# Kernel tuning notes

Hardware: AMD Instinct MI355X
Metric: run time of the kernel (lower is better)

## Reference

```python
import jax, jax.numpy as jnp
import numpy as np

GROUP_SIZE = 128  # K-rows sharing one dequant scale


def _dequant(B, s):
    """Unpack int4 (uint4b8: value = nibble - 8) from packed int32 and apply group scales.
    B: [K//8, N] int32, 8 nibbles per word along K (nibble i -> k = 8*row + i).
    s: [K//GROUP_SIZE, N] float scales.
    Returns W: [K, N] float.
    """
    Kp, N = B.shape
    K = Kp * 8
    shifts = (jnp.arange(8, dtype=jnp.int32) * 4)
    # [Kp, 8, N] nibbles -> [K, N]
    nib = (B[:, None, :] >> shifts[None, :, None]) & 0xF
    w = nib.reshape(K, N).astype(s.dtype) - 8.0
    # per-group scaling: groups of GROUP_SIZE consecutive K rows
    w = (w.reshape(K // GROUP_SIZE, GROUP_SIZE, N) * s[:, None, :]).reshape(K, N)
    return w


def setup_inputs() -> dict:
    key = jax.random.key(0)
    k1, k2, k3 = jax.random.split(key, 3)
    M, K, N = 64, 8192, 8192
    x = jax.random.normal(k1, (M, K), dtype=jnp.float32)
    B = jax.random.randint(k2, (K // 8, N), 0, 2147483647, dtype=jnp.int32)
    s = jax.random.uniform(k3, (K // GROUP_SIZE, N), dtype=jnp.float32) * 0.02
    return {"x": x, "B": B, "s": s}


def reference(x, B, s):
    # machete_mm: fused int4 dequant + GEMM; here expressed as dequant then matmul
    w = _dequant(B, s)          # [K, N]
    out = x @ w                 # [M, N]
    return out
```

## Files before the change

kernel.cpp:

```cpp
#include <hip/hip_runtime.h>

typedef _Float16 half2v __attribute__((ext_vector_type(2)));
typedef _Float16 half8  __attribute__((ext_vector_type(8)));
typedef float    floatx4 __attribute__((ext_vector_type(4)));

#define M_DIM 64
#define K_DIM 8192
#define N_DIM 8192
#define NT 64
#define KSPLIT 4

__global__ __launch_bounds__(256) void permute_x_kernel(
        const float* __restrict__ x, _Float16* __restrict__ xp) {
    int t = blockIdx.x * 256 + threadIdx.x;
    const float* src = x + (size_t)t * 8;
    float4 a = *(const float4*)(src);
    float4 b = *(const float4*)(src + 4);
    union { _Float16 h[8]; float4 f; } u;
    u.h[0] = (_Float16)a.x; u.h[1] = (_Float16)b.x;
    u.h[2] = (_Float16)a.y; u.h[3] = (_Float16)b.y;
    u.h[4] = (_Float16)a.z; u.h[5] = (_Float16)b.z;
    u.h[6] = (_Float16)a.w; u.h[7] = (_Float16)b.w;
    *(float4*)(xp + (size_t)t * 8) = u.f;
}

__device__ __forceinline__ half2v dq_pair(unsigned int bits, half2v sub, half2v sc) {
    union { unsigned int u; half2v h; } cv;
    cv.u = bits;
    return (cv.h - sub) * sc;
}

__global__ __launch_bounds__(256, 2) void machete_mm_kernel(
        const _Float16* __restrict__ xp,
        const unsigned int* __restrict__ Bq,
        const float* __restrict__ s,
        float* __restrict__ out) {
    __shared__ float red[4][M_DIM][NT];

    const int tid  = threadIdx.x;
    const int w    = tid >> 6;
    const int lane = tid & 63;
    const int c    = lane & 15;
    const int q    = lane >> 4;
    const int n0   = blockIdx.x * NT;
    const int ci   = blockIdx.y * 4 + w;
    const int kb   = ci * (K_DIM / (KSPLIT * 4));

    const int ncol = n0 + 4 * c;

    floatx4 acc[4][4];
    #pragma unroll
    for (int i = 0; i < 4; ++i)
        #pragma unroll
        for (int j = 0; j < 4; ++j) acc[i][j] = (floatx4)0.0f;

    const unsigned int* bptr = Bq + (size_t)((kb >> 3) + q) * N_DIM + ncol;
    const _Float16*     aptr = xp + (size_t)c * K_DIM + kb + q * 8;

    const half2v c1032 = { (_Float16)1032.0f, (_Float16)1032.0f };

    #pragma unroll
    for (int g = 0; g < 4; ++g) {
        const int gg = (kb >> 7) + g;
        const float4 s4 = *(const float4*)(s + (size_t)gg * N_DIM + ncol);
        half2v s2[4];
        s2[0] = (half2v){ (_Float16)s4.x, (_Float16)s4.x };
        s2[1] = (half2v){ (_Float16)s4.y, (_Float16)s4.y };
        s2[2] = (half2v){ (_Float16)s4.z, (_Float16)s4.z };
        s2[3] = (half2v){ (_Float16)s4.w, (_Float16)s4.w };

        #pragma unroll
        for (int st = 0; st < 4; ++st) {
            half8 afr[4];
            #pragma unroll
            for (int mt = 0; mt < 4; ++mt)
                afr[mt] = *(const half8*)(aptr + (size_t)mt * 16 * K_DIM);

            union { uint4 v; unsigned int a[4]; } bv;
            bv.v = *(const uint4*)bptr;

            #pragma unroll
            for (int t = 0; t < 4; ++t) {
                const unsigned int wd = bv.a[t];
                union { half2v h2[4]; half8 h8; } bf;
                bf.h2[0] = dq_pair(( wd        & 0x000F000Fu) | 0x64006400u, c1032, s2[t]);
                bf.h2[1] = dq_pair(((wd >> 4)  & 0x000F000Fu) | 0x64006400u, c1032, s2[t]);
                bf.h2[2] = dq_pair(((wd >> 8)  & 0x000F000Fu) | 0x64006400u, c1032, s2[t]);
                bf.h2[3] = dq_pair(((wd >> 12) & 0x000F000Fu) | 0x64006400u, c1032, s2[t]);
                #pragma unroll
                for (int mt = 0; mt < 4; ++mt)
                    acc[mt][t] = __builtin_amdgcn_mfma_f32_16x16x32_f16(
                        afr[mt], bf.h8, acc[mt][t], 0, 0, 0);
            }
            aptr += 32;
            bptr += (size_t)4 * N_DIM;
        }
    }

    #pragma unroll
    for (int mt = 0; mt < 4; ++mt)
        #pragma unroll
        for (int t = 0; t < 4; ++t)
            #pragma unroll
            for (int r = 0; r < 4; ++r)
                red[w][mt * 16 + q * 4 + r][4 * c + t] = acc[mt][t][r];
    __syncthreads();

    #pragma unroll
    for (int i = 0; i < 16; ++i) {
        int idx = i * 256 + tid;
        int m = idx >> 6, nl = idx & 63;
        float v = red[0][m][nl] + red[1][m][nl] + red[2][m][nl] + red[3][m][nl];
        atomicAdd(out + (size_t)m * N_DIM + n0 + nl, v);
    }
}

extern "C" void kernel_launch(void* const* d_in, const int* in_sizes, int n_in,
                              void* d_out, int out_size, void* d_ws, size_t ws_size,
                              hipStream_t stream) {
    const float*        x  = (const float*)d_in[0];
    const unsigned int* Bq = (const unsigned int*)d_in[1];
    const float*        sc = (const float*)d_in[2];
    float* out    = (float*)d_out;
    _Float16* xp  = (_Float16*)d_ws;

    hipMemsetAsync(d_out, 0, (size_t)M_DIM * N_DIM * sizeof(float), stream);
    permute_x_kernel<<<dim3((M_DIM * K_DIM / 8) / 256), 256, 0, stream>>>(x, xp);
    machete_mm_kernel<<<dim3(N_DIM / NT, KSPLIT), 256, 0, stream>>>(xp, Bq, sc, out);
}
```

Before: 101.2 us.

## Software-pipeline B/A loads and replace atomic split-K with partial buffer reduction

The main loop is flattened into 16 steps, with B words prefetched two steps ahead through a triple buffer and A fragments prefetched one step ahead. This hides global load latency behind the MFMA and dequant work. The atomicAdd split-K epilogue and the output memset are replaced by plain stores of per-split partials into workspace, followed by a separate reduce kernel. The shared reduction buffer is halved and padded, which lowers LDS use and bank conflicts but adds an extra launch and partial-buffer traffic.

```diff
diff --git a/kernel.cpp b/kernel.cpp
--- a/kernel.cpp
+++ b/kernel.cpp
@@ -8,7 +8,7 @@
 #define K_DIM 8192
 #define N_DIM 8192
 #define NT 64
-#define KSPLIT 4
+#define KSB 4
 
 __global__ __launch_bounds__(256) void permute_x_kernel(
         const float* __restrict__ x, _Float16* __restrict__ xp) {
@@ -34,8 +34,8 @@
         const _Float16* __restrict__ xp,
         const unsigned int* __restrict__ Bq,
         const float* __restrict__ s,
-        float* __restrict__ out) {
-    __shared__ float red[4][M_DIM][NT];
+        float* __restrict__ partial) {
+    __shared__ float red[4][32][65];
 
     const int tid  = threadIdx.x;
     const int w    = tid >> 6;
@@ -44,7 +44,7 @@
     const int q    = lane >> 4;
     const int n0   = blockIdx.x * NT;
     const int ci   = blockIdx.y * 4 + w;
-    const int kb   = ci * (K_DIM / (KSPLIT * 4));
+    const int kb   = ci * (K_DIM / (KSB * 4));
 
     const int ncol = n0 + 4 * c;
 
@@ -54,65 +54,99 @@
         #pragma unroll
         for (int j = 0; j < 4; ++j) acc[i][j] = (floatx4)0.0f;
 
+    const half2v c1032 = { (_Float16)1032.0f, (_Float16)1032.0f };
+    half2v s2g[4][4];
+    #pragma unroll
+    for (int g = 0; g < 4; ++g) {
+        const float4 s4 = *(const float4*)(s + (size_t)((kb >> 7) + g) * N_DIM + ncol);
+        s2g[g][0] = (half2v){ (_Float16)s4.x, (_Float16)s4.x };
+        s2g[g][1] = (half2v){ (_Float16)s4.y, (_Float16)s4.y };
+        s2g[g][2] = (half2v){ (_Float16)s4.z, (_Float16)s4.z };
+        s2g[g][3] = (half2v){ (_Float16)s4.w, (_Float16)s4.w };
+    }
+
     const unsigned int* bptr = Bq + (size_t)((kb >> 3) + q) * N_DIM + ncol;
     const _Float16*     aptr = xp + (size_t)c * K_DIM + kb + q * 8;
 
-    const half2v c1032 = { (_Float16)1032.0f, (_Float16)1032.0f };
+    uint4 bbuf[3];
+    half8 abuf[2][4];
+    bbuf[0] = *(const uint4*)bptr; bptr += (size_t)4 * N_DIM;
+    bbuf[1] = *(const uint4*)bptr; bptr += (size_t)4 * N_DIM;
+    #pragma unroll
+    for (int mt = 0; mt < 4; ++mt)
+        abuf[0][mt] = *(const half8*)(aptr + (size_t)mt * 16 * K_DIM);
 
     #pragma unroll
-    for (int g = 0; g < 4; ++g) {
-        const int gg = (kb >> 7) + g;
-        const float4 s4 = *(const float4*)(s + (size_t)gg * N_DIM + ncol);
-        half2v s2[4];
-        s2[0] = (half2v){ (_Float16)s4.x, (_Float16)s4.x };
-        s2[1] = (half2v){ (_Float16)s4.y, (_Float16)s4.y };
-        s2[2] = (half2v){ (_Float16)s4.z, (_Float16)s4.z };
-        s2[3] = (half2v){ (_Float16)s4.w, (_Float16)s4.w };
+    for (int st = 0; st < 16; ++st) {
+        if (st < 14) {
+            bbuf[(st + 2) % 3] = *(const uint4*)bptr;
+            bptr += (size_t)4 * N_DIM;
+        }
+        if (st < 15) {
+            #pragma unroll
+            for (int mt = 0; mt < 4; ++mt)
+                abuf[(st + 1) & 1][mt] =
+                    *(const half8*)(aptr + 32 + (size_t)mt * 16 * K_DIM);
+        }
+
+        union { uint4 v; unsigned int a[4]; } bv;
+        bv.v = bbuf[st % 3];
+        const int g = st >> 2;
 
         #pragma unroll
-        for (int st = 0; st < 4; ++st) {
-            half8 afr[4];
+        for (int t = 0; t < 4; ++t) {
+            const unsigned int wd = bv.a[t];
+            const half2v sc = s2g[g][t];
+            union { half2v h2[4]; half8 h8; } bf;
+            bf.h2[0] = dq_pair(( wd        & 0x000F000Fu) | 0x64006400u, c1032, sc);
+            bf.h2[1] = dq_pair(((wd >> 4)  & 0x000F000Fu) | 0x64006400u, c1032, sc);
+            bf.h2[2] = dq_pair(((wd >> 8)  & 0x000F000Fu) | 0x64006400u, c1032, sc);
+            bf.h2[3] = dq_pair(((wd >> 12) & 0x000F000Fu) | 0x64006400u, c1032, sc);
             #pragma unroll
             for (int mt = 0; mt < 4; ++mt)
-                afr[mt] = *(const half8*)(aptr + (size_t)mt * 16 * K_DIM);
+                acc[mt][t] = __builtin_amdgcn_mfma_f32_16x16x32_f16(
+                    abuf[st & 1][mt], bf.h8, acc[mt][t], 0, 0, 0);
+        }
+        aptr += 32;
+    }
 
-            union { uint4 v; unsigned int a[4]; } bv;
-            bv.v = *(const uint4*)bptr;
-
+    float* ptile = partial + ((size_t)blockIdx.y * M_DIM) * N_DIM + n0;
+    #pragma unroll
+    for (int r = 0; r < 2; ++r) {
+        if (r) __syncthreads();
+        #pragma unroll
+        for (int h = 0; h < 2; ++h) {
+            const int mt = 2 * r + h;
             #pragma unroll
-            for (int t = 0; t < 4; ++t) {
-                const unsigned int wd = bv.a[t];
-                union { half2v h2[4]; half8 h8; } bf;
-                bf.h2[0] = dq_pair(( wd        & 0x000F000Fu) | 0x64006400u, c1032, s2[t]);
-                bf.h2[1] = dq_pair(((wd >> 4)  & 0x000F000Fu) | 0x64006400u, c1032, s2[t]);
-                bf.h2[2] = dq_pair(((wd >> 8)  & 0x000F000Fu) | 0x64006400u, c1032, s2[t]);
-                bf.h2[3] = dq_pair(((wd >> 12) & 0x000F000Fu) | 0x64006400u, c1032, s2[t]);
+            for (int t = 0; t < 4; ++t)
                 #pragma unroll
-                for (int mt = 0; mt < 4; ++mt)
-                    acc[mt][t] = __builtin_amdgcn_mfma_f32_16x16x32_f16(
-                        afr[mt], bf.h8, acc[mt][t], 0, 0, 0);
-            }
-            aptr += 32;
-            bptr += (size_t)4 * N_DIM;
+                for (int rr = 0; rr < 4; ++rr)
+                    red[w][h * 16 + q * 4 + rr][4 * c + t] = acc[mt][t][rr];
+        }
+        __syncthreads();
+        #pragma unroll
+        for (int i = 0; i < 8; ++i) {
+            const int idx = i * 256 + tid;
+            const int mr  = idx >> 6;
+            const int nl  = idx & 63;
+            const float v = red[0][mr][nl] + red[1][mr][nl]
+                          + red[2][mr][nl] + red[3][mr][nl];
+            ptile[(size_t)(r * 32 + mr) * N_DIM + nl] = v;
         }
     }
+}
 
+__global__ __launch_bounds__(256) void reduce_kernel(
+        const float* __restrict__ partial, float* __restrict__ out) {
+    const size_t i = ((size_t)blockIdx.x * 256 + threadIdx.x) * 4;
+    const size_t S = (size_t)M_DIM * N_DIM;
+    float4 v = *(const float4*)(partial + i);
     #pragma unroll
-    for (int mt = 0; mt < 4; ++mt)
-        #pragma unroll
-        for (int t = 0; t < 4; ++t)
-            #pragma unroll
-            for (int r = 0; r < 4; ++r)
-                red[w][mt * 16 + q * 4 + r][4 * c + t] = acc[mt][t][r];
-    __syncthreads();
-
-    #pragma unroll
-    for (int i = 0; i < 16; ++i) {
-        int idx = i * 256 + tid;
-        int m = idx >> 6, nl = idx & 63;
-        float v = red[0][m][nl] + red[1][m][nl] + red[2][m][nl] + red[3][m][nl];
-        atomicAdd(out + (size_t)m * N_DIM + n0 + nl, v);
+    for (int bk = 1; bk < KSB; ++bk) {
+        const float4 u = *(const float4*)(partial + bk * S + i);
+        v.x += u.x; v.y += u.y; v.z += u.z; v.w += u.w;
     }
+    *(float4*)(out + i) = v;
 }
 
 extern "C" void kernel_launch(void* const* d_in, const int* in_sizes, int n_in,
@@ -121,10 +155,11 @@
     const float*        x  = (const float*)d_in[0];
     const unsigned int* Bq = (const unsigned int*)d_in[1];
     const float*        sc = (const float*)d_in[2];
-    float* out    = (float*)d_out;
-    _Float16* xp  = (_Float16*)d_ws;
+    float* out     = (float*)d_out;
+    _Float16* xp   = (_Float16*)d_ws;
+    float* partial = (float*)((char*)d_ws + (1 << 20));
 
-    hipMemsetAsync(d_out, 0, (size_t)M_DIM * N_DIM * sizeof(float), stream);
     permute_x_kernel<<<dim3((M_DIM * K_DIM / 8) / 256), 256, 0, stream>>>(x, xp);
-    machete_mm_kernel<<<dim3(N_DIM / NT, KSPLIT), 256, 0, stream>>>(xp, Bq, sc, out);
+    machete_mm_kernel<<<dim3(N_DIM / NT, KSB), 256, 0, stream>>>(xp, Bq, sc, partial);
+    reduce_kernel<<<dim3(M_DIM * N_DIM / (256 * 4)), 256, 0, stream>>>(partial, out);
 }
```

Measured after the change: 104.2 us. 3.0% more time.
